# Kernel tuning notes

Measured on AMD Instinct MI355X. Metric: run time of the kernel, lower is better.

Reference implementation:

```python
import jax, jax.numpy as jnp
import numpy as np
import math

B, S, E, H = 2, 2048, 1024, 16
HD = E // H          # head_dim = 64
HX = 64              # helix_dim
P = HX // 2          # helix pairs = 32

def setup_inputs() -> dict:
    key = jax.random.key(0)
    ks = jax.random.split(key, 12)
    sc = 0.02
    return {
        "x":    jax.random.normal(ks[0], (B, S, E), dtype=jnp.float32),
        "Wq":   jax.random.normal(ks[1], (E, E), dtype=jnp.float32) * sc,
        "bq":   jnp.zeros((E,), dtype=jnp.float32),
        "Wk":   jax.random.normal(ks[2], (E, E), dtype=jnp.float32) * sc,
        "bk":   jnp.zeros((E,), dtype=jnp.float32),
        "Wv":   jax.random.normal(ks[3], (E, E), dtype=jnp.float32) * sc,
        "bv":   jnp.zeros((E,), dtype=jnp.float32),
        "Wo":   jax.random.normal(ks[4], (E, E), dtype=jnp.float32) * sc,
        "bo":   jnp.zeros((E,), dtype=jnp.float32),
        "Whel": jax.random.normal(ks[5], (H, HX, HD), dtype=jnp.float32) * sc,
        "bhel": jnp.zeros((H, HX), dtype=jnp.float32),
    }

def _l2norm(x, eps=1e-12):
    # torch F.normalize(p=2, dim=-1): x / max(||x||, eps)
    n = jnp.sqrt(jnp.sum(x * x, axis=-1, keepdims=True))
    return x / jnp.maximum(n, eps)

def _scramble(t):
    # faithful to torch: (B,S,2) -> transpose(1,2) -> reshape(B,S,2),
    # vectorized over (H,P): t is (B,H,P,S,2)
    b, h, p, s, _ = t.shape
    return jnp.swapaxes(t, -1, -2).reshape(b, h, p, s, 2)

def reference(x, Wq, bq, Wk, bk, Wv, bv, Wo, bo, Whel, bhel):
    b, s, e = x.shape
    h, hx, hd = Whel.shape
    p = hx // 2
    q = x @ Wq.T + bq
    k = x @ Wk.T + bk
    v = x @ Wv.T + bv
    qh = q.reshape(b, s, h, hd)
    kh = k.reshape(b, s, h, hd)
    # per-head helical projections: (B,S,H,HX)
    q_hel = jnp.einsum('bshd,hed->bshe', qh, Whel) + bhel
    k_hel = jnp.einsum('bshd,hed->bshe', kh, Whel) + bhel
    # split into 2D coords, normalize each pair: (B,H,P,S,2)
    qn = _l2norm(q_hel.reshape(b, s, h, p, 2)).transpose(0, 2, 3, 1, 4)
    kn = _l2norm(k_hel.reshape(b, s, h, p, 2)).transpose(0, 2, 3, 1, 4)
    qn = _scramble(qn)
    kn = _scramble(kn)
    # helical similarity averaged over pairs: (B,H,S,S)
    helical = jnp.einsum('bhpsc,bhptc->bhst', qn, kn) / p
    # standard scaled dot-product scores
    dot = jnp.einsum('bshd,bthd->bhst', qh, kh) / math.sqrt(hd)
    alpha = 0.5
    attn = jax.nn.softmax(alpha * dot + (1.0 - alpha) * helical, axis=-1)
    vh = v.reshape(b, s, h, hd)
    out = jnp.einsum('bhst,bthd->bshd', attn, vh).reshape(b, s, e)
    return out @ Wo.T + bo
```

## Files before the change

kernel.cpp:

```cpp
#include <hip/hip_runtime.h>
#include <hip/hip_bf16.h>


typedef unsigned short u16;
typedef unsigned int u32;
typedef __attribute__((ext_vector_type(8))) __bf16 bf16x8;
typedef __attribute__((ext_vector_type(4))) float f32x4;

__device__ __forceinline__ u16 f2b(float f) {
  u32 u = __float_as_uint(f);
  u32 r = (u + 0x7fffu + ((u >> 16) & 1u)) >> 16;
  return (u16)r;
}
__device__ __forceinline__ float b2f(u16 h) {
  return __uint_as_float(((u32)h) << 16);
}

__device__ __forceinline__ f32x4 mfma16(bf16x8 a, bf16x8 b, f32x4 c) {
  return __builtin_amdgcn_mfma_f32_16x16x32_bf16(a, b, c, 0, 0, 0);
}

__device__ __forceinline__ void gld16(void* lds, const void* g) {
  __builtin_amdgcn_global_load_lds(
      (const __attribute__((address_space(1))) unsigned int*)g,
      (__attribute__((address_space(3))) unsigned int*)lds, 16, 0, 0);
}

__global__ __launch_bounds__(256) void cast_kernel(
    const float* __restrict__ x,  const float* __restrict__ wq,
    const float* __restrict__ wk, const float* __restrict__ wv,
    const float* __restrict__ wo, const float* __restrict__ whel,
    u16* __restrict__ xb, u16* __restrict__ wb, u16* __restrict__ wob,
    u16* __restrict__ whb) {
  long long q = (long long)blockIdx.x * 256 + threadIdx.x;
  const float* s; u16* d; long long base;
  if (q < 1048576)      { s = x;    d = xb;            base = 0; }
  else if (q < 1310720) { s = wq;   d = wb;            base = 1048576; }
  else if (q < 1572864) { s = wk;   d = wb + 1048576;  base = 1310720; }
  else if (q < 1835008) { s = wv;   d = wb + 2097152;  base = 1572864; }
  else if (q < 2097152) { s = wo;   d = wob;           base = 1835008; }
  else                  { s = whel; d = whb;           base = 2097152; }
  long long e = (q - base) * 4;
  float4 v = *(const float4*)(s + e);
  ushort4 o;
  o.x = f2b(v.x); o.y = f2b(v.y); o.z = f2b(v.z); o.w = f2b(v.w);
  *(ushort4*)(d + e) = o;
}

__global__ __launch_bounds__(256, 2) void qkv_gemm(
    const u16* __restrict__ xb, const u16* __restrict__ wb,
    const float* __restrict__ bq, const float* __restrict__ bk,
    const float* __restrict__ bv,
    u16* __restrict__ Qcat, u16* __restrict__ Kcat, u16* __restrict__ vt) {
  __shared__ u16 Al[128][32];
  __shared__ u16 Bl[128][32];
  __shared__ u16 T[64][136];
  const int nt = blockIdx.x, mt = blockIdx.y;
  const int which = nt >> 3;
  const int n0 = (nt & 7) << 7;
  const int m0 = mt << 7;
  const int tid = threadIdx.x;
  const int wave = tid >> 6, lane = tid & 63;
  const int g = lane >> 4, c15 = lane & 15;
  const int wm = wave & 1, wn = wave >> 1;
  const u16* Wp = wb + (long long)which * (1024 * 1024) + n0 * 1024;
  const u16* Ap = xb + m0 * 1024;
  const int srow = (wave * 64 + lane) >> 2;
  const int scol = (lane & 3) << 3;

  f32x4 acc[4][4];
#pragma unroll
  for (int i = 0; i < 4; i++)
#pragma unroll
    for (int j = 0; j < 4; j++) acc[i][j] = f32x4{0.f, 0.f, 0.f, 0.f};

  for (int k0 = 0; k0 < 1024; k0 += 32) {
    gld16(&Al[srow][scol],      Ap + srow * 1024 + k0 + scol);
    gld16(&Al[64 + srow][scol], Ap + (64 + srow) * 1024 + k0 + scol);
    gld16(&Bl[srow][scol],      Wp + srow * 1024 + k0 + scol);
    gld16(&Bl[64 + srow][scol], Wp + (64 + srow) * 1024 + k0 + scol);
    __syncthreads();
    bf16x8 a[4], b[4];
#pragma unroll
    for (int i = 0; i < 4; i++)
      a[i] = *(const bf16x8*)&Al[wm * 64 + i * 16 + c15][g * 8];
#pragma unroll
    for (int j = 0; j < 4; j++)
      b[j] = *(const bf16x8*)&Bl[wn * 64 + j * 16 + c15][g * 8];
#pragma unroll
    for (int i = 0; i < 4; i++)
#pragma unroll
      for (int j = 0; j < 4; j++) acc[i][j] = mfma16(a[i], b[j], acc[i][j]);
    __syncthreads();
  }

  if (which == 2) {
#pragma unroll
    for (int half = 0; half < 2; ++half) {
      __syncthreads();
      if (wn == half) {
#pragma unroll
        for (int i = 0; i < 4; i++)
#pragma unroll
          for (int j = 0; j < 4; j++)
#pragma unroll
            for (int r = 0; r < 4; r++) {
              int nloc = j * 16 + c15;
              int mloc = wm * 64 + i * 16 + g * 4 + r;
              float v = acc[i][j][r] + bv[n0 + half * 64 + nloc];
              T[nloc][mloc] = f2b(v);
            }
      }
      __syncthreads();
#pragma unroll
      for (int it = 0; it < 4; ++it) {
        int idx = it * 256 + tid;
        int row = idx >> 4;
        int cm = (idx & 15) * 8;
        int col = n0 + half * 64 + row;
        int hh = col >> 6, dd = col & 63;
        int m = m0 + cm;
        int bb2 = m >> 11, s = m & 2047;
        *(uint4*)&vt[(((bb2 * 16 + hh) * 64) + dd) * 2048 + s] =
            *(const uint4*)&T[row][cm];
      }
    }
    return;
  }

  const float* bias = (which == 0) ? bq : bk;
#pragma unroll
  for (int i = 0; i < 4; i++)
#pragma unroll
    for (int j = 0; j < 4; j++)
#pragma unroll
      for (int r = 0; r < 4; r++) {
        int row = m0 + wm * 64 + i * 16 + g * 4 + r;
        int col = n0 + wn * 64 + j * 16 + c15;
        float v = acc[i][j][r] + bias[col];
        int bb = row >> 11, s = row & 2047;
        int hh = col >> 6, d = col & 63;
        if (which == 0) {
          Qcat[(((bb * 16 + hh) * 2048) + s) * 128 + d] = f2b(v * 0.0625f);
        } else {
          Kcat[(((bb * 16 + hh) * 2048) + s) * 128 + d] = f2b(v);
        }
      }
}

__global__ __launch_bounds__(256, 2) void helical_kernel(
    u16* __restrict__ Qcat, u16* __restrict__ Kcat,
    const u16* __restrict__ whb, const float* __restrict__ bhel) {
  __shared__ u16 A[2][2][64][32];
  __shared__ u16 Wl[2][64][32];
  const int sb = blockIdx.x, bh = blockIdx.y;
  const int h = bh & 15;
  const int s0 = sb << 6;
  const int tid = threadIdx.x;
  const int wave = tid >> 6, lane = tid & 63;
  const int g = lane >> 4, c15 = lane & 15;
  u16* Qb = Qcat + (long long)bh * (2048 * 128);
  u16* Kb = Kcat + (long long)bh * (2048 * 128);

#pragma unroll
  for (int it = 0; it < 2; ++it) {
    int cidx = it * 256 + tid;
    int e = cidx >> 3, ds = (cidx & 7) << 3;
    uint4 vv = *(const uint4*)(whb + h * 4096 + e * 64 + ds);
    *(uint4*)&Wl[ds >> 5][e][ds & 31] = vv;
  }
#pragma unroll
  for (int it = 0; it < 4; ++it) {
    int cidx = it * 256 + tid;
    int which = cidx >> 9;
    int r = (cidx >> 3) & 63;
    int ds = (cidx & 7) << 3;
    const u16* src = (which ? Kb : Qb) + (s0 + r) * 128 + ds;
    uint4 vv = *(const uint4*)src;
    if (which == 0) {
      u16 tmp[8];
      *(uint4*)tmp = vv;
#pragma unroll
      for (int q = 0; q < 8; ++q) tmp[q] = f2b(b2f(tmp[q]) * 16.0f);
      vv = *(uint4*)tmp;
    }
    *(uint4*)&A[which][ds >> 5][r][ds & 31] = vv;
  }
  __syncthreads();

  const int which = wave >> 1, hf = wave & 1;
  f32x4 acc[2][4];
#pragma unroll
  for (int i = 0; i < 2; i++)
#pragma unroll
    for (int j = 0; j < 4; j++) acc[i][j] = f32x4{0.f, 0.f, 0.f, 0.f};
#pragma unroll
  for (int kq = 0; kq < 2; ++kq) {
    bf16x8 a0 = *(const bf16x8*)&A[which][kq][hf * 32 + c15][g * 8];
    bf16x8 a1 = *(const bf16x8*)&A[which][kq][hf * 32 + 16 + c15][g * 8];
#pragma unroll
    for (int j = 0; j < 4; ++j) {
      bf16x8 bb = *(const bf16x8*)&Wl[kq][j * 16 + c15][g * 8];
      acc[0][j] = mfma16(a0, bb, acc[0][j]);
      acc[1][j] = mfma16(a1, bb, acc[1][j]);
    }
  }
  u16* Dst = which ? Kb : Qb;
#pragma unroll
  for (int i = 0; i < 2; ++i)
#pragma unroll
    for (int j = 0; j < 4; ++j)
#pragma unroll
      for (int r = 0; r < 4; ++r) {
        int s_loc = hf * 32 + i * 16 + g * 4 + r;
        int e = j * 16 + c15;
        float v = acc[i][j][r] + bhel[h * 64 + e];
        float pp = __shfl_xor(v, 1);
        float nn = sqrtf(v * v + pp * pp);
        float o = v / fmaxf(nn, 1e-12f) * 0.125f;
        int s = s0 + s_loc;
        int u = s >> 1, c2 = s & 1;
        int row_out = ((e & 1) ? 1024 : 0) + u;
        int col_out = 64 + (e & ~1) + c2;
        Dst[row_out * 128 + col_out] = f2b(o);
      }
}

__global__ __launch_bounds__(256, 4) void attn_kernel(
    const u16* __restrict__ Qcat, const u16* __restrict__ Kcat,
    const u16* __restrict__ vt, u16* __restrict__ AO) {
  __shared__ u16 Kl[4][64][32];
  __shared__ u16 Vl[2][64][32];
  __shared__ u16 Pl[2][64][40];
  const int qt = blockIdx.x, bh = blockIdx.y;
  const int bb = bh >> 4, h = bh & 15;
  const int q0 = qt << 6;
  const int tid = threadIdx.x;
  const int wave = tid >> 6, lane = tid & 63;
  const int g = lane >> 4, c15 = lane & 15;
  const u16* Qb = Qcat + (long long)bh * (2048 * 128);
  const u16* Kb = Kcat + (long long)bh * (2048 * 128);
  const u16* Vb = vt + (long long)bh * (64 * 2048);
  const int r4 = (wave * 64 + lane) >> 2;
  const int c8 = (lane & 3) << 3;
  const int lin8 = (wave * 64 + lane) * 8;

  bf16x8 qf[4];
#pragma unroll
  for (int kq = 0; kq < 4; ++kq)
    qf[kq] = *(const bf16x8*)(Qb + (q0 + wave * 16 + c15) * 128 + kq * 32 +
                              g * 8);

  f32x4 accO[4];
  float den[4];
#pragma unroll
  for (int j = 0; j < 4; j++) accO[j] = f32x4{0.f, 0.f, 0.f, 0.f};
#pragma unroll
  for (int r = 0; r < 4; r++) den[r] = 0.f;

  for (int t = 0; t < 32; ++t) {
    const int t0 = t << 6;
#pragma unroll
    for (int kq = 0; kq < 4; ++kq)
      gld16(((u16*)Kl) + kq * 2048 + lin8, Kb + (t0 + r4) * 128 + kq * 32 + c8);
#pragma unroll
    for (int tq = 0; tq < 2; ++tq)
      gld16(((u16*)Vl) + tq * 2048 + lin8, Vb + r4 * 2048 + t0 + tq * 32 + c8);
    __syncthreads();

    f32x4 accS[4];
#pragma unroll
    for (int j = 0; j < 4; j++) accS[j] = f32x4{0.f, 0.f, 0.f, 0.f};
#pragma unroll
    for (int kq = 0; kq < 4; ++kq) {
#pragma unroll
      for (int j = 0; j < 4; ++j) {
        bf16x8 bk2 = *(const bf16x8*)&Kl[kq][j * 16 + c15][g * 8];
        accS[j] = mfma16(qf[kq], bk2, accS[j]);
      }
    }

#pragma unroll
    for (int j = 0; j < 4; ++j) {
      int tq = j >> 1;
      int tc = ((j & 1) << 4) + c15;
      int mrow = wave * 16 + g * 4;
#pragma unroll
      for (int r = 0; r < 4; ++r) {
        float p = __expf(accS[j][r]);
        den[r] += p;
        Pl[tq][mrow + r][tc] = (u16)(__float_as_uint(p) >> 16);
      }
    }

#pragma unroll
    for (int tq = 0; tq < 2; ++tq) {
      bf16x8 a = *(const bf16x8*)&Pl[tq][wave * 16 + c15][g * 8];
#pragma unroll
      for (int j = 0; j < 4; ++j) {
        bf16x8 bv2 = *(const bf16x8*)&Vl[tq][j * 16 + c15][g * 8];
        accO[j] = mfma16(a, bv2, accO[j]);
      }
    }
    __syncthreads();
  }

#pragma unroll
  for (int r = 0; r < 4; ++r) {
    float v = den[r];
    v += __shfl_xor(v, 1);
    v += __shfl_xor(v, 2);
    v += __shfl_xor(v, 4);
    v += __shfl_xor(v, 8);
    den[r] = v;
  }

#pragma unroll
  for (int j = 0; j < 4; ++j)
#pragma unroll
    for (int r = 0; r < 4; ++r) {
      int s = q0 + wave * 16 + g * 4 + r;
      float o = accO[j][r] / den[r];
      int d = j * 16 + c15;
      AO[((bb * 2048 + s) * 1024) + h * 64 + d] = f2b(o);
    }
}

__global__ __launch_bounds__(256, 2) void out_gemm(
    const u16* __restrict__ AO, const u16* __restrict__ wob,
    const float* __restrict__ bo, float* __restrict__ out) {
  __shared__ u16 Al[128][32];
  __shared__ u16 Bl[128][32];
  const int n0 = blockIdx.x << 7;
  const int m0 = blockIdx.y << 7;
  const int tid = threadIdx.x;
  const int wave = tid >> 6, lane = tid & 63;
  const int g = lane >> 4, c15 = lane & 15;
  const int wm = wave & 1, wn = wave >> 1;
  const u16* Wp = wob + n0 * 1024;
  const u16* Ap = AO + m0 * 1024;
  const int srow = (wave * 64 + lane) >> 2;
  const int scol = (lane & 3) << 3;

  f32x4 acc[4][4];
#pragma unroll
  for (int i = 0; i < 4; i++)
#pragma unroll
    for (int j = 0; j < 4; j++) acc[i][j] = f32x4{0.f, 0.f, 0.f, 0.f};

  for (int k0 = 0; k0 < 1024; k0 += 32) {
    gld16(&Al[srow][scol],      Ap + srow * 1024 + k0 + scol);
    gld16(&Al[64 + srow][scol], Ap + (64 + srow) * 1024 + k0 + scol);
    gld16(&Bl[srow][scol],      Wp + srow * 1024 + k0 + scol);
    gld16(&Bl[64 + srow][scol], Wp + (64 + srow) * 1024 + k0 + scol);
    __syncthreads();
    bf16x8 a[4], b[4];
#pragma unroll
    for (int i = 0; i < 4; i++)
      a[i] = *(const bf16x8*)&Al[wm * 64 + i * 16 + c15][g * 8];
#pragma unroll
    for (int j = 0; j < 4; j++)
      b[j] = *(const bf16x8*)&Bl[wn * 64 + j * 16 + c15][g * 8];
#pragma unroll
    for (int i = 0; i < 4; i++)
#pragma unroll
      for (int j = 0; j < 4; j++) acc[i][j] = mfma16(a[i], b[j], acc[i][j]);
    __syncthreads();
  }
#pragma unroll
  for (int i = 0; i < 4; i++)
#pragma unroll
    for (int j = 0; j < 4; j++)
#pragma unroll
      for (int r = 0; r < 4; r++) {
        int row = m0 + wm * 64 + i * 16 + g * 4 + r;
        int col = n0 + wn * 64 + j * 16 + c15;
        out[row * 1024 + col] = acc[i][j][r] + bo[col];
      }
}

extern "C" void kernel_launch(void* const* d_in, const int* in_sizes, int n_in,
                              void* d_out, int out_size, void* d_ws,
                              size_t ws_size, hipStream_t stream) {
  const float* x    = (const float*)d_in[0];
  const float* Wq   = (const float*)d_in[1];
  const float* bq   = (const float*)d_in[2];
  const float* Wk   = (const float*)d_in[3];
  const float* bk   = (const float*)d_in[4];
  const float* Wv   = (const float*)d_in[5];
  const float* bv   = (const float*)d_in[6];
  const float* Wo   = (const float*)d_in[7];
  const float* bo   = (const float*)d_in[8];
  const float* Whel = (const float*)d_in[9];
  const float* bhel = (const float*)d_in[10];
  float* out = (float*)d_out;

  char* ws = (char*)d_ws;
  u16* xb   = (u16*)(ws + 0);
  u16* wb   = (u16*)(ws + 8388608);
  u16* wob  = (u16*)(ws + 14680064);
  u16* whb  = (u16*)(ws + 16777216);
  u16* Qcat = (u16*)(ws + 16908288);
  u16* Kcat = (u16*)(ws + 33685504);
  u16* vt   = (u16*)(ws + 50462720);
  u16* AO   = (u16*)(ws + 58851328);

  dim3 blk(256);
  cast_kernel<<<dim3(8256), blk, 0, stream>>>(x, Wq, Wk, Wv, Wo, Whel, xb, wb,
                                              wob, whb);
  qkv_gemm<<<dim3(24, 32), blk, 0, stream>>>(xb, wb, bq, bk, bv, Qcat, Kcat,
                                             vt);
  helical_kernel<<<dim3(32, 32), blk, 0, stream>>>(Qcat, Kcat, whb, bhel);
  attn_kernel<<<dim3(32, 32), blk, 0, stream>>>(Qcat, Kcat, vt, AO);
  out_gemm<<<dim3(8, 32), blk, 0, stream>>>(AO, wob, bo, out);
}
```

Baseline: 254.6 us.

## Rewrite attention kernel with 32x32 MFMA, swizzled LDS, and exp2 softmax

Restructures the attention inner loop to use 32x32x16 bf16 MFMAs, splitting the four waves into a 2x2 grid over query and key tiles. S is computed transposed as K·Q so P can be written to LDS, and a per-row denominator is reduced through shared memory at the end. K and V tiles are loaded into LDS with an XOR swizzle to cut bank conflicts. The log2(e) factor is folded into the Q scaling upstream so the softmax can use the hardware exp2 instruction. The cost is an extra __syncthreads per tile and more complex indexing.

```diff
diff --git a/kernel.cpp b/kernel.cpp
--- a/kernel.cpp
+++ b/kernel.cpp
@@ -6,6 +6,7 @@
 typedef unsigned int u32;
 typedef __attribute__((ext_vector_type(8))) __bf16 bf16x8;
 typedef __attribute__((ext_vector_type(4))) float f32x4;
+typedef __attribute__((ext_vector_type(16))) float f32x16;
 
 __device__ __forceinline__ u16 f2b(float f) {
   u32 u = __float_as_uint(f);
@@ -19,12 +20,17 @@
 __device__ __forceinline__ f32x4 mfma16(bf16x8 a, bf16x8 b, f32x4 c) {
   return __builtin_amdgcn_mfma_f32_16x16x32_bf16(a, b, c, 0, 0, 0);
 }
+__device__ __forceinline__ f32x16 mfma32(bf16x8 a, bf16x8 b, f32x16 c) {
+  return __builtin_amdgcn_mfma_f32_32x32x16_bf16(a, b, c, 0, 0, 0);
+}
 
 __device__ __forceinline__ void gld16(void* lds, const void* g) {
   __builtin_amdgcn_global_load_lds(
       (const __attribute__((address_space(1))) unsigned int*)g,
       (__attribute__((address_space(3))) unsigned int*)lds, 16, 0, 0);
 }
+
+#define LOG2E 1.4426950408889634f
 
 __global__ __launch_bounds__(256) void cast_kernel(
     const float* __restrict__ x,  const float* __restrict__ wq,
@@ -141,7 +147,8 @@
         int bb = row >> 11, s = row & 2047;
         int hh = col >> 6, d = col & 63;
         if (which == 0) {
-          Qcat[(((bb * 16 + hh) * 2048) + s) * 128 + d] = f2b(v * 0.0625f);
+          Qcat[(((bb * 16 + hh) * 2048) + s) * 128 + d] =
+              f2b(v * (0.0625f * LOG2E));
         } else {
           Kcat[(((bb * 16 + hh) * 2048) + s) * 128 + d] = f2b(v);
         }
@@ -181,7 +188,8 @@
       u16 tmp[8];
       *(uint4*)tmp = vv;
 #pragma unroll
-      for (int q = 0; q < 8; ++q) tmp[q] = f2b(b2f(tmp[q]) * 16.0f);
+      for (int q = 0; q < 8; ++q)
+        tmp[q] = f2b(b2f(tmp[q]) * (16.0f / LOG2E));
       vv = *(uint4*)tmp;
     }
     *(uint4*)&A[which][ds >> 5][r][ds & 31] = vv;
@@ -206,6 +214,7 @@
     }
   }
   u16* Dst = which ? Kb : Qb;
+  const float oscale = which ? 0.125f : (0.125f * LOG2E);
 #pragma unroll
   for (int i = 0; i < 2; ++i)
 #pragma unroll
@@ -217,7 +226,7 @@
         float v = acc[i][j][r] + bhel[h * 64 + e];
         float pp = __shfl_xor(v, 1);
         float nn = sqrtf(v * v + pp * pp);
-        float o = v / fmaxf(nn, 1e-12f) * 0.125f;
+        float o = v / fmaxf(nn, 1e-12f) * oscale;
         int s = s0 + s_loc;
         int u = s >> 1, c2 = s & 1;
         int row_out = ((e & 1) ? 1024 : 0) + u;
@@ -231,99 +240,108 @@
     const u16* __restrict__ vt, u16* __restrict__ AO) {
   __shared__ u16 Kl[4][64][32];
   __shared__ u16 Vl[2][64][32];
-  __shared__ u16 Pl[2][64][40];
+  __shared__ u16 Pl[64][68];
+  __shared__ float denl[2][64];
   const int qt = blockIdx.x, bh = blockIdx.y;
   const int bb = bh >> 4, h = bh & 15;
   const int q0 = qt << 6;
   const int tid = threadIdx.x;
-  const int wave = tid >> 6, lane = tid & 63;
-  const int g = lane >> 4, c15 = lane & 15;
+  const int w = tid >> 6, lane = tid & 63;
+  const int wq = w & 1, wt = w >> 1;
+  const int l31 = lane & 31, l5 = lane >> 5;
   const u16* Qb = Qcat + (long long)bh * (2048 * 128);
   const u16* Kb = Kcat + (long long)bh * (2048 * 128);
   const u16* Vb = vt + (long long)bh * (64 * 2048);
-  const int r4 = (wave * 64 + lane) >> 2;
-  const int c8 = (lane & 3) << 3;
-  const int lin8 = (wave * 64 + lane) * 8;
-
-  bf16x8 qf[4];
-#pragma unroll
-  for (int kq = 0; kq < 4; ++kq)
-    qf[kq] = *(const bf16x8*)(Qb + (q0 + wave * 16 + c15) * 128 + kq * 32 +
-                              g * 8);
-
-  f32x4 accO[4];
-  float den[4];
-#pragma unroll
-  for (int j = 0; j < 4; j++) accO[j] = f32x4{0.f, 0.f, 0.f, 0.f};
-#pragma unroll
-  for (int r = 0; r < 4; r++) den[r] = 0.f;
+
+  const int srow = lane >> 2;
+  const int sc = lane & 3;
+
+  bf16x8 qf[8];
+  {
+    const u16* qrow = Qb + (q0 + 32 * wq + l31) * 128 + l5 * 8;
+#pragma unroll
+    for (int ks = 0; ks < 8; ++ks) qf[ks] = *(const bf16x8*)(qrow + ks * 16);
+  }
+
+  f32x16 accO;
+#pragma unroll
+  for (int i = 0; i < 16; ++i) accO[i] = 0.f;
+  float den = 0.f;
 
   for (int t = 0; t < 32; ++t) {
     const int t0 = t << 6;
 #pragma unroll
-    for (int kq = 0; kq < 4; ++kq)
-      gld16(((u16*)Kl) + kq * 2048 + lin8, Kb + (t0 + r4) * 128 + kq * 32 + c8);
-#pragma unroll
-    for (int tq = 0; tq < 2; ++tq)
-      gld16(((u16*)Vl) + tq * 2048 + lin8, Vb + r4 * 2048 + t0 + tq * 32 + c8);
-    __syncthreads();
-
-    f32x4 accS[4];
-#pragma unroll
-    for (int j = 0; j < 4; j++) accS[j] = f32x4{0.f, 0.f, 0.f, 0.f};
-#pragma unroll
-    for (int kq = 0; kq < 4; ++kq) {
-#pragma unroll
-      for (int j = 0; j < 4; ++j) {
-        bf16x8 bk2 = *(const bf16x8*)&Kl[kq][j * 16 + c15][g * 8];
-        accS[j] = mfma16(qf[kq], bk2, accS[j]);
-      }
-    }
-
-#pragma unroll
-    for (int j = 0; j < 4; ++j) {
-      int tq = j >> 1;
-      int tc = ((j & 1) << 4) + c15;
-      int mrow = wave * 16 + g * 4;
-#pragma unroll
-      for (int r = 0; r < 4; ++r) {
-        float p = __expf(accS[j][r]);
-        den[r] += p;
-        Pl[tq][mrow + r][tc] = (u16)(__float_as_uint(p) >> 16);
-      }
-    }
-
-#pragma unroll
-    for (int tq = 0; tq < 2; ++tq) {
-      bf16x8 a = *(const bf16x8*)&Pl[tq][wave * 16 + c15][g * 8];
-#pragma unroll
-      for (int j = 0; j < 4; ++j) {
-        bf16x8 bv2 = *(const bf16x8*)&Vl[tq][j * 16 + c15][g * 8];
-        accO[j] = mfma16(a, bv2, accO[j]);
-      }
-    }
-    __syncthreads();
-  }
-
-#pragma unroll
-  for (int r = 0; r < 4; ++r) {
-    float v = den[r];
-    v += __shfl_xor(v, 1);
-    v += __shfl_xor(v, 2);
-    v += __shfl_xor(v, 4);
-    v += __shfl_xor(v, 8);
-    den[r] = v;
-  }
-
-#pragma unroll
-  for (int j = 0; j < 4; ++j)
-#pragma unroll
-    for (int r = 0; r < 4; ++r) {
-      int s = q0 + wave * 16 + g * 4 + r;
-      float o = accO[j][r] / den[r];
-      int d = j * 16 + c15;
-      AO[((bb * 2048 + s) * 1024) + h * 64 + d] = f2b(o);
-    }
+    for (int rg = 0; rg < 4; ++rg) {
+      int row = rg * 16 + srow;
+      int cc = sc ^ ((row >> 1) & 3);
+      gld16(((u16*)Kl) + w * 2048 + rg * 512 + lane * 8,
+            Kb + (t0 + row) * 128 + w * 32 + cc * 8);
+    }
+    {
+      int drow = w * 16 + srow;
+      int cc = sc ^ ((drow >> 1) & 3);
+#pragma unroll
+      for (int tq = 0; tq < 2; ++tq)
+        gld16(((u16*)Vl) + tq * 2048 + w * 512 + lane * 8,
+              Vb + drow * 2048 + t0 + tq * 32 + cc * 8);
+    }
+    __syncthreads();
+
+    f32x16 accS;
+#pragma unroll
+    for (int i = 0; i < 16; ++i) accS[i] = 0.f;
+    {
+      const int row = 32 * wt + l31;
+      const int sw = (row >> 1) & 3;
+#pragma unroll
+      for (int ks = 0; ks < 8; ++ks) {
+        int cp = (2 * (ks & 1) + l5) ^ sw;
+        bf16x8 ak = *(const bf16x8*)&Kl[ks >> 1][row][cp * 8];
+        accS = mfma32(ak, qf[ks], accS);
+      }
+    }
+
+#pragma unroll
+    for (int rr = 0; rr < 4; ++rr) {
+      u16 pk[4];
+#pragma unroll
+      for (int r2 = 0; r2 < 4; ++r2) {
+        float p = __builtin_amdgcn_exp2f(accS[rr * 4 + r2]);
+        den += p;
+        pk[r2] = (u16)(__float_as_uint(p) >> 16);
+      }
+      *(uint2*)&Pl[32 * wq + l31][32 * wt + 8 * rr + 4 * l5] =
+          *(const uint2*)pk;
+    }
+    __syncthreads();
+
+    {
+      const int drow = 32 * wt + l31;
+      const int sw = (drow >> 1) & 3;
+#pragma unroll
+      for (int ks = 0; ks < 4; ++ks) {
+        bf16x8 ap = *(const bf16x8*)&Pl[32 * wq + l31][ks * 16 + l5 * 8];
+        int ct = 2 * ks + l5;
+        bf16x8 bvf = *(const bf16x8*)&Vl[ct >> 2][drow][((ct & 3) ^ sw) * 8];
+        accO = mfma32(ap, bvf, accO);
+      }
+    }
+    __syncthreads();
+  }
+
+  den += __shfl_xor(den, 32);
+  if (lane < 32) denl[wt][32 * wq + lane] = den;
+  __syncthreads();
+
+#pragma unroll
+  for (int r = 0; r < 16; ++r) {
+    int q_loc = 32 * wq + (r & 3) + 8 * (r >> 2) + 4 * l5;
+    float dfull = denl[0][q_loc] + denl[1][q_loc];
+    float o = accO[r] / dfull;
+    int q = q0 + q_loc;
+    int d = h * 64 + 32 * wt + l31;
+    AO[((bb * 2048 + q) * 1024) + d] = f2b(o);
+  }
 }
 
 __global__ __launch_bounds__(256, 2) void out_gemm(
```

Result: faster. 236.0 us (-7.3%).
